# Optimization experiments

Hardware: AMD Instinct MI355X
Metric: run time of the kernel (lower is better)

Reference implementation:

```python
import jax, jax.numpy as jnp
import numpy as np
from jax import lax

# Fixed LBP neighbor-difference filters: each of 8 filters is (neighbor - center)
_LBP_W = np.array([
    [[[0,0,1],[0,-1,0],[0,0,0]]],
    [[[0,0,0],[0,-1,1],[0,0,0]]],
    [[[0,0,0],[0,-1,0],[0,0,1]]],
    [[[0,0,0],[0,-1,0],[0,1,0]]],
    [[[0,0,0],[0,-1,0],[1,0,0]]],
    [[[0,0,0],[1,-1,0],[0,0,0]]],
    [[[1,0,0],[0,-1,0],[0,0,0]]],
    [[[0,1,0],[0,-1,0],[0,0,0]]],
], dtype=np.float32)  # [8,1,3,3] OIHW

_RGB2GRAY = np.array([0.299, 0.587, 0.114], dtype=np.float32)


def setup_inputs() -> dict:
    key = jax.random.key(0)
    img = jax.random.uniform(key, (16, 3, 1024, 1024), dtype=jnp.float32)
    lbp_weight = jnp.asarray(_LBP_W)                                   # [8,1,3,3]
    kernel_weight = jnp.asarray(2.0 ** np.arange(8, dtype=np.float32)  # 1,2,...,128
                                ).reshape(1, 8, 1, 1)
    return {"img": img, "lbp_weight": lbp_weight, "kernel_weight": kernel_weight}


def reference(img, lbp_weight, kernel_weight):
    # rgb2gray: [B,3,H,W] -> [B,1,H,W]
    gray = jnp.einsum("bchw,c->bhw", img, jnp.asarray(_RGB2GRAY))[:, None]
    # 3x3 LBP neighbor-difference conv, padding=1 (SAME)
    out = lax.conv_general_dilated(
        gray, lbp_weight, window_strides=(1, 1), padding=((1, 1), (1, 1)),
        dimension_numbers=("NCHW", "OIHW", "NCHW"))                    # [B,8,H,W]
    # threshold then weighted sum of bit-planes -> LBP code in [0,255]
    bits = jnp.where(out >= 0.0, 1.0, 0.0)
    lbp_img = jnp.sum(bits * kernel_weight, axis=1)                     # [B,H,W]
    # 256-bin histogram over ALL elements (matches torch.where counting loop)
    idx = lbp_img.astype(jnp.int32).reshape(-1)
    hist = jnp.zeros((1, 256), dtype=jnp.float32).at[0, idx].add(1.0)
    # standardize with unbiased std (torch.std default, ddof=1)
    mean = jnp.mean(hist, axis=1, keepdims=True)
    std = jnp.sqrt(jnp.sum((hist - mean) ** 2, axis=1, keepdims=True) / (256 - 1))
    return (hist - mean) / std
```

## Files before the change

### kernel.cpp

```cpp
#include <hip/hip_runtime.h>

#define TX 64
#define TY 32
#define HALO_W (TX + 2)
#define HALO_H (TY + 2)
#define NTX (1024 / TX)
#define NTY (1024 / TY)
#define NBATCH 16
#define NTILES (NTX * NTY * NBATCH)
#define NBLOCKS 2048

__global__ void lbp_zero_hist(unsigned* __restrict__ g_hist) {
    g_hist[threadIdx.x] = 0u;
}

__global__ __launch_bounds__(256) void lbp_hist_kernel(
        const float* __restrict__ img, unsigned* __restrict__ g_hist) {
    __shared__ float tile[HALO_H][HALO_W];
    __shared__ unsigned s_hist[256];
    const int tid = threadIdx.x;
    s_hist[tid] = 0u;

    for (int t = blockIdx.x; t < NTILES; t += NBLOCKS) {
        const int bx  = t % NTX;
        const int rem = t / NTX;
        const int by  = rem % NTY;
        const int b   = rem / NTY;
        const int x0 = bx * TX - 1;
        const int y0 = by * TY - 1;
        const float* imgb = img + (size_t)b * 3u * 1024u * 1024u;

        __syncthreads();
        for (int idx = tid; idx < HALO_H * HALO_W; idx += 256) {
            const int ly = idx / HALO_W;
            const int lx = idx - ly * HALO_W;
            const int gy = y0 + ly;
            const int gx = x0 + lx;
            float gval = 0.0f;
            if ((unsigned)gy < 1024u && (unsigned)gx < 1024u) {
                const size_t off = (size_t)gy * 1024u + (size_t)gx;
                const float r = imgb[off];
                const float g = imgb[off + 1024u * 1024u];
                const float bb = imgb[off + 2u * 1024u * 1024u];
                gval = (r * 0.299f + g * 0.587f) + bb * 0.114f;
            }
            tile[ly][lx] = gval;
        }
        __syncthreads();

        const int tx  = tid & 63;
        const int ty0 = tid >> 6;
        #pragma unroll
        for (int rr = 0; rr < TY / 4; ++rr) {
            const int ly = ty0 + 4 * rr;
            const float c = tile[ly + 1][tx + 1];
            unsigned code =
                (tile[ly    ][tx + 2] >= c ? 1u   : 0u) |
                (tile[ly + 1][tx + 2] >= c ? 2u   : 0u) |
                (tile[ly + 2][tx + 2] >= c ? 4u   : 0u) |
                (tile[ly + 2][tx + 1] >= c ? 8u   : 0u) |
                (tile[ly + 2][tx    ] >= c ? 16u  : 0u) |
                (tile[ly + 1][tx    ] >= c ? 32u  : 0u) |
                (tile[ly    ][tx    ] >= c ? 64u  : 0u) |
                (tile[ly    ][tx + 1] >= c ? 128u : 0u);
            atomicAdd(&s_hist[code], 1u);
        }
    }
    __syncthreads();
    atomicAdd(&g_hist[tid], s_hist[tid]);
}

__global__ __launch_bounds__(256) void lbp_finalize(
        const unsigned* __restrict__ g_hist, float* __restrict__ out) {
    __shared__ float red[256];
    const int i = threadIdx.x;
    const float h = (float)g_hist[i];
    red[i] = h;
    __syncthreads();
    #pragma unroll
    for (int s = 128; s > 0; s >>= 1) {
        if (i < s) red[i] += red[i + s];
        __syncthreads();
    }
    const float mean = red[0] * (1.0f / 256.0f);
    __syncthreads();
    const float d = h - mean;
    red[i] = d * d;
    __syncthreads();
    #pragma unroll
    for (int s = 128; s > 0; s >>= 1) {
        if (i < s) red[i] += red[i + s];
        __syncthreads();
    }
    const float stdv = sqrtf(red[0] * (1.0f / 255.0f));
    out[i] = d / stdv;
}

extern "C" void kernel_launch(void* const* d_in, const int* in_sizes, int n_in,
                              void* d_out, int out_size, void* d_ws, size_t ws_size,
                              hipStream_t stream) {
    const float* img = (const float*)d_in[0];
    unsigned* g_hist = (unsigned*)d_ws;
    float* out = (float*)d_out;

    lbp_zero_hist<<<1, 256, 0, stream>>>(g_hist);
    lbp_hist_kernel<<<NBLOCKS, 256, 0, stream>>>(img, g_hist);
    lbp_finalize<<<1, 256, 0, stream>>>(g_hist, out);
}
```

Baseline: 308.2 us.

## Vectorize tile loads, slide 3x3 window in registers, privatize histograms

```diff
diff --git a/kernel.cpp b/kernel.cpp
--- a/kernel.cpp
+++ b/kernel.cpp
@@ -2,79 +2,110 @@
 
 #define TX 64
 #define TY 32
-#define HALO_W (TX + 2)
-#define HALO_H (TY + 2)
+#define TILE_H 34
+#define TILE_W 72
 #define NTX (1024 / TX)
 #define NTY (1024 / TY)
 #define NBATCH 16
 #define NTILES (NTX * NTY * NBATCH)
 #define NBLOCKS 2048
+#define NHIST 8
 
 __global__ void lbp_zero_hist(unsigned* __restrict__ g_hist) {
-    g_hist[threadIdx.x] = 0u;
+    g_hist[blockIdx.x * 256 + threadIdx.x] = 0u;
 }
 
 __global__ __launch_bounds__(256) void lbp_hist_kernel(
         const float* __restrict__ img, unsigned* __restrict__ g_hist) {
-    __shared__ float tile[HALO_H][HALO_W];
-    __shared__ unsigned s_hist[256];
+    __shared__ __align__(16) float tile[TILE_H][TILE_W];
+    __shared__ unsigned s_hist[4][256];
     const int tid = threadIdx.x;
-    s_hist[tid] = 0u;
+    const int wv  = tid >> 6;
+    #pragma unroll
+    for (int w = 0; w < 4; ++w) s_hist[w][tid] = 0u;
+
+    const int tx = tid & 63;
+    const int ry = wv * 8;
 
     for (int t = blockIdx.x; t < NTILES; t += NBLOCKS) {
         const int bx  = t % NTX;
         const int rem = t / NTX;
         const int by  = rem % NTY;
         const int b   = rem / NTY;
-        const int x0 = bx * TX - 1;
-        const int y0 = by * TY - 1;
+        const int y0  = by * TY - 1;
+        const int xq0 = bx * TX - 4;
         const float* imgb = img + (size_t)b * 3u * 1024u * 1024u;
 
         __syncthreads();
-        for (int idx = tid; idx < HALO_H * HALO_W; idx += 256) {
-            const int ly = idx / HALO_W;
-            const int lx = idx - ly * HALO_W;
-            const int gy = y0 + ly;
-            const int gx = x0 + lx;
-            float gval = 0.0f;
-            if ((unsigned)gy < 1024u && (unsigned)gx < 1024u) {
-                const size_t off = (size_t)gy * 1024u + (size_t)gx;
-                const float r = imgb[off];
-                const float g = imgb[off + 1024u * 1024u];
-                const float bb = imgb[off + 2u * 1024u * 1024u];
-                gval = (r * 0.299f + g * 0.587f) + bb * 0.114f;
+
+        for (int it = tid; it < TILE_H * 18; it += 256) {
+            const int row = it / 18;
+            const int q   = it - row * 18;
+            const int gy  = y0 + row;
+            const int gxq = xq0 + (q << 2);
+            float4 gv = make_float4(0.f, 0.f, 0.f, 0.f);
+            if ((unsigned)gy < 1024u) {
+                const float* rowp = imgb + (size_t)gy * 1024u;
+                if ((unsigned)gxq <= 1020u) {
+                    const float4 r4 = *(const float4*)(rowp + gxq);
+                    const float4 g4 = *(const float4*)(rowp + 1048576u + gxq);
+                    const float4 b4 = *(const float4*)(rowp + 2097152u + gxq);
+                    gv.x = (r4.x * 0.299f + g4.x * 0.587f) + b4.x * 0.114f;
+                    gv.y = (r4.y * 0.299f + g4.y * 0.587f) + b4.y * 0.114f;
+                    gv.z = (r4.z * 0.299f + g4.z * 0.587f) + b4.z * 0.114f;
+                    gv.w = (r4.w * 0.299f + g4.w * 0.587f) + b4.w * 0.114f;
+                } else {
+                    #pragma unroll
+                    for (int k = 0; k < 4; ++k) {
+                        const int gx = gxq + k;
+                        if ((unsigned)gx < 1024u) {
+                            const float r  = rowp[gx];
+                            const float g  = rowp[1048576u + gx];
+                            const float bb = rowp[2097152u + gx];
+                            ((float*)&gv)[k] = (r * 0.299f + g * 0.587f) + bb * 0.114f;
+                        }
+                    }
+                }
             }
-            tile[ly][lx] = gval;
+            *(float4*)&tile[row][q << 2] = gv;
         }
         __syncthreads();
 
-        const int tx  = tid & 63;
-        const int ty0 = tid >> 6;
+        float c00 = tile[ry    ][tx + 3], c01 = tile[ry    ][tx + 4], c02 = tile[ry    ][tx + 5];
+        float c10 = tile[ry + 1][tx + 3], c11 = tile[ry + 1][tx + 4], c12 = tile[ry + 1][tx + 5];
         #pragma unroll
-        for (int rr = 0; rr < TY / 4; ++rr) {
-            const int ly = ty0 + 4 * rr;
-            const float c = tile[ly + 1][tx + 1];
-            unsigned code =
-                (tile[ly    ][tx + 2] >= c ? 1u   : 0u) |
-                (tile[ly + 1][tx + 2] >= c ? 2u   : 0u) |
-                (tile[ly + 2][tx + 2] >= c ? 4u   : 0u) |
-                (tile[ly + 2][tx + 1] >= c ? 8u   : 0u) |
-                (tile[ly + 2][tx    ] >= c ? 16u  : 0u) |
-                (tile[ly + 1][tx    ] >= c ? 32u  : 0u) |
-                (tile[ly    ][tx    ] >= c ? 64u  : 0u) |
-                (tile[ly    ][tx + 1] >= c ? 128u : 0u);
-            atomicAdd(&s_hist[code], 1u);
+        for (int p = 0; p < 8; ++p) {
+            const float c20 = tile[ry + p + 2][tx + 3];
+            const float c21 = tile[ry + p + 2][tx + 4];
+            const float c22 = tile[ry + p + 2][tx + 5];
+            const unsigned code =
+                (c02 >= c11 ? 1u   : 0u) |
+                (c12 >= c11 ? 2u   : 0u) |
+                (c22 >= c11 ? 4u   : 0u) |
+                (c21 >= c11 ? 8u   : 0u) |
+                (c20 >= c11 ? 16u  : 0u) |
+                (c10 >= c11 ? 32u  : 0u) |
+                (c00 >= c11 ? 64u  : 0u) |
+                (c01 >= c11 ? 128u : 0u);
+            atomicAdd(&s_hist[wv][code], 1u);
+            c00 = c10; c01 = c11; c02 = c12;
+            c10 = c20; c11 = c21; c12 = c22;
         }
     }
+
     __syncthreads();
-    atomicAdd(&g_hist[tid], s_hist[tid]);
+    const unsigned total = s_hist[0][tid] + s_hist[1][tid] + s_hist[2][tid] + s_hist[3][tid];
+    atomicAdd(&g_hist[((blockIdx.x & (NHIST - 1)) << 8) + tid], total);
 }
 
 __global__ __launch_bounds__(256) void lbp_finalize(
         const unsigned* __restrict__ g_hist, float* __restrict__ out) {
     __shared__ float red[256];
     const int i = threadIdx.x;
-    const float h = (float)g_hist[i];
+    unsigned hv = 0u;
+    #pragma unroll
+    for (int c = 0; c < NHIST; ++c) hv += g_hist[(c << 8) + i];
+    const float h = (float)hv;
     red[i] = h;
     __syncthreads();
     #pragma unroll
@@ -103,7 +134,7 @@
     unsigned* g_hist = (unsigned*)d_ws;
     float* out = (float*)d_out;
 
-    lbp_zero_hist<<<1, 256, 0, stream>>>(g_hist);
+    lbp_zero_hist<<<NHIST, 256, 0, stream>>>(g_hist);
     lbp_hist_kernel<<<NBLOCKS, 256, 0, stream>>>(img, g_hist);
     lbp_finalize<<<1, 256, 0, stream>>>(g_hist, out);
 }
```

New measurement: 284.5 us. -7.7%, faster.
